# Performance work log

Measured on AMD Instinct MI355X. Metric: run time of the kernel, lower is better.

The kernel has to match this reference:

```python
import jax, jax.numpy as jnp
import numpy as np

D_HID = 1024
N_HEADS = 16
D_HEAD = D_HID // N_HEADS


def setup_inputs() -> dict:
    key = jax.random.key(0)
    k_x, k_w, k_b = jax.random.split(key, 3)
    x = jax.random.normal(k_x, (8, 4096, D_HID), dtype=jnp.float32)
    # qkv linear params (torch Linear: y = x @ W.T + b; we store W already transposed)
    W_qkv = jax.random.normal(k_w, (D_HID, 3 * D_HID), dtype=jnp.float32) / np.sqrt(D_HID)
    b_qkv = jax.random.normal(k_b, (3 * D_HID,), dtype=jnp.float32) * 0.01
    return {"x": x, "W_qkv": W_qkv, "b_qkv": b_qkv}


def reference(x, W_qkv, b_qkv):
    B, N, _ = x.shape
    qkv = x @ W_qkv + b_qkv  # [B, N, 3*d_hid]
    q, k, v = jnp.split(qkv, 3, axis=-1)

    def heads(t):  # [B, N, d_hid] -> [B, H, N, d_head]
        return t.reshape(B, N, N_HEADS, D_HEAD).transpose(0, 2, 1, 3)

    q, k, v = heads(q), heads(k), heads(v)
    # channel attention: contract over sequence N -> [B, H, d_head, d_head]
    attn = jnp.einsum("bhnd,bhne->bhde", q, k) / np.sqrt(D_HEAD)
    attn = jax.nn.softmax(attn, axis=-1)  # softmax over channel dim
    # outputs = V @ attn : [B, H, N, d_head]
    out = jnp.einsum("bhnd,bhde->bhne", v, attn)
    out = out.transpose(0, 2, 1, 3).reshape(B, N, N_HEADS * D_HEAD)
    return out
```

## Files before the change

### kernel.cpp

```cpp
#include <hip/hip_runtime.h>
#include <hip/hip_bf16.h>


typedef __attribute__((ext_vector_type(4))) float  f32x4;
typedef __attribute__((ext_vector_type(8))) short  bf16x8;
typedef __attribute__((ext_vector_type(8))) unsigned short u16x8;

typedef __attribute__((address_space(1))) const unsigned int GBUF;
typedef __attribute__((address_space(3))) unsigned int       LBUF;

#define DEVI __device__ __forceinline__

static constexpr int BATCH = 8;
static constexpr int NSEQ  = 4096;
static constexpr int DHID  = 1024;
static constexpr int NHEAD = 16;
static constexpr int DH    = 64;
static constexpr int MROWS = BATCH * NSEQ;
static constexpr int N3    = 3 * DHID;

DEVI unsigned short f2bf(float f) {
    unsigned int u = __float_as_uint(f);
    u = (u + 0x7fffu + ((u >> 16) & 1u)) >> 16;
    return (unsigned short)u;
}

__global__ void k_cvt_x(const float* __restrict__ x, unsigned short* __restrict__ xb, int n8) {
    int i = blockIdx.x * 256 + threadIdx.x;
    int stride = gridDim.x * 256;
    for (; i < n8; i += stride) {
        f32x4 a = *(const f32x4*)(x + (size_t)i * 8);
        f32x4 b = *(const f32x4*)(x + (size_t)i * 8 + 4);
        u16x8 r;
#pragma unroll
        for (int j = 0; j < 4; j++) { r[j] = f2bf(a[j]); r[4 + j] = f2bf(b[j]); }
        *(u16x8*)(xb + (size_t)i * 8) = r;
    }
}

__global__ void k_wt(const float* __restrict__ W, unsigned short* __restrict__ Wt) {
    __shared__ float s[32][33];
    int c0 = blockIdx.x * 32;
    int k0 = blockIdx.y * 32;
    int tx = threadIdx.x & 31, ty = threadIdx.x >> 5;
#pragma unroll
    for (int i = 0; i < 4; i++)
        s[ty + 8 * i][tx] = W[(size_t)(k0 + ty + 8 * i) * N3 + c0 + tx];
    __syncthreads();
#pragma unroll
    for (int i = 0; i < 4; i++)
        Wt[(size_t)(c0 + ty + 8 * i) * DHID + k0 + tx] = f2bf(s[tx][ty + 8 * i]);
}

__global__ __launch_bounds__(256, 2) void k_gemm1(
        const unsigned short* __restrict__ xb, const unsigned short* __restrict__ Wt,
        const float* __restrict__ bias,
        unsigned short* __restrict__ Q, unsigned short* __restrict__ Kw,
        unsigned short* __restrict__ V) {
    __shared__ unsigned short As[128 * 32];
    __shared__ unsigned short Bs[128 * 32];

    int nwg = gridDim.x;
    int cpx = nwg >> 3;
    int id  = blockIdx.x;
    int swz = (id & 7) * cpx + (id >> 3);
    int mt = swz / 24, nt = swz % 24;
    int m0 = mt * 128, n0 = nt * 128;

    int t = threadIdx.x, l = t & 63, w = t >> 6;
    int wr = w >> 1, wc = w & 1;

    const unsigned short* aSrc = xb + (size_t)m0 * DHID;
    const unsigned short* bSrc = Wt + (size_t)n0 * DHID;
    int srow  = l >> 2;
    int skoff = (l & 3) * 8;

    f32x4 acc[4][4] = {};

    for (int ks = 0; ks < 32; ks++) {
        int kk = ks * 32;
#pragma unroll
        for (int i = 0; i < 2; i++) {
            int r = w * 32 + i * 16 + srow;
            __builtin_amdgcn_global_load_lds(
                (GBUF*)(aSrc + (size_t)r * DHID + kk + skoff),
                (LBUF*)((char*)As + (w * 2 + i) * 1024), 16, 0, 0);
            __builtin_amdgcn_global_load_lds(
                (GBUF*)(bSrc + (size_t)r * DHID + kk + skoff),
                (LBUF*)((char*)Bs + (w * 2 + i) * 1024), 16, 0, 0);
        }
        __syncthreads();
        bf16x8 af[4], bfr[4];
#pragma unroll
        for (int m = 0; m < 4; m++)
            af[m] = *(const bf16x8*)(As + (wr * 64 + m * 16 + (l & 15)) * 32 + (l >> 4) * 8);
#pragma unroll
        for (int n = 0; n < 4; n++)
            bfr[n] = *(const bf16x8*)(Bs + (wc * 64 + n * 16 + (l & 15)) * 32 + (l >> 4) * 8);
#pragma unroll
        for (int m = 0; m < 4; m++)
#pragma unroll
            for (int n = 0; n < 4; n++)
                acc[m][n] = __builtin_amdgcn_mfma_f32_16x16x32_bf16(af[m], bfr[n], acc[m][n], 0, 0, 0);
        __syncthreads();
    }

    int hg   = (n0 + wc * 64) >> 6;
    int part = hg >> 4;
    int h    = hg & 15;
    unsigned short* dst = (part == 0) ? Q : ((part == 1) ? Kw : V);
    int b   = m0 >> 12;
    int nnb = m0 & 4095;
    unsigned short* dstp = dst + ((size_t)(b * 16 + h) * NSEQ) * DH;

#pragma unroll
    for (int n = 0; n < 4; n++) {
        int e   = n * 16 + (l & 15);
        float bv = bias[n0 + wc * 64 + n * 16 + (l & 15)];
#pragma unroll
        for (int m = 0; m < 4; m++) {
            int r0 = nnb + wr * 64 + m * 16 + (l >> 4) * 4;
#pragma unroll
            for (int j = 0; j < 4; j++)
                dstp[(size_t)(r0 + j) * DH + e] = f2bf(acc[m][n][j] + bv);
        }
    }
}

__global__ __launch_bounds__(256, 2) void k_qk(
        const unsigned short* __restrict__ Q, const unsigned short* __restrict__ K,
        float* __restrict__ part) {
    __shared__ unsigned short Qt[64 * 40];
    __shared__ unsigned short Kt[64 * 40];

    int bid = blockIdx.x;
    int bh = bid >> 2, ch = bid & 3;
    const unsigned short* Qb = Q + ((size_t)bh * NSEQ + ch * 1024) * DH;
    const unsigned short* Kb = K + ((size_t)bh * NSEQ + ch * 1024) * DH;

    int t = threadIdx.x, l = t & 63, w = t >> 6;
    int wr = w >> 1, wc = w & 1;
    int nn = t & 31;
    int dg = t >> 5;

    f32x4 acc[2][2] = {};

    for (int ns = 0; ns < 32; ns++) {
        const size_t ro = (size_t)(ns * 32 + nn) * DH + dg * 8;
        bf16x8 qv = *(const bf16x8*)(Qb + ro);
        bf16x8 kv = *(const bf16x8*)(Kb + ro);
        __syncthreads();
#pragma unroll
        for (int j = 0; j < 8; j++) {
            Qt[(dg * 8 + j) * 40 + nn] = qv[j];
            Kt[(dg * 8 + j) * 40 + nn] = kv[j];
        }
        __syncthreads();
        bf16x8 a[2], b[2];
#pragma unroll
        for (int m = 0; m < 2; m++)
            a[m] = *(const bf16x8*)(Qt + (wr * 32 + m * 16 + (l & 15)) * 40 + (l >> 4) * 8);
#pragma unroll
        for (int n = 0; n < 2; n++)
            b[n] = *(const bf16x8*)(Kt + (wc * 32 + n * 16 + (l & 15)) * 40 + (l >> 4) * 8);
#pragma unroll
        for (int m = 0; m < 2; m++)
#pragma unroll
            for (int n = 0; n < 2; n++)
                acc[m][n] = __builtin_amdgcn_mfma_f32_16x16x32_bf16(a[m], b[n], acc[m][n], 0, 0, 0);
    }

    float* P = part + ((size_t)ch * 128 + bh) * 4096;
#pragma unroll
    for (int m = 0; m < 2; m++)
#pragma unroll
        for (int n = 0; n < 2; n++)
#pragma unroll
            for (int j = 0; j < 4; j++) {
                int d = wr * 32 + m * 16 + (l >> 4) * 4 + j;
                int e = wc * 32 + n * 16 + (l & 15);
                P[d * 64 + e] = acc[m][n][j];
            }
}

__global__ void k_softmax(const float* __restrict__ part, unsigned short* __restrict__ attn_t) {
    int bh = blockIdx.x;
    int d  = threadIdx.x;
    const float* p = part + (size_t)bh * 4096 + d * 64;
    const size_t cs = (size_t)128 * 4096;
    float s[64];
#pragma unroll
    for (int e = 0; e < 64; e++)
        s[e] = (p[e] + p[cs + e] + p[2 * cs + e] + p[3 * cs + e]) * 0.125f;
    float mx = s[0];
#pragma unroll
    for (int e = 1; e < 64; e++) mx = fmaxf(mx, s[e]);
    float sum = 0.f;
#pragma unroll
    for (int e = 0; e < 64; e++) { s[e] = __expf(s[e] - mx); sum += s[e]; }
    float inv = 1.f / sum;
    unsigned short* a = attn_t + (size_t)bh * 4096;
#pragma unroll
    for (int e = 0; e < 64; e++)
        a[e * 64 + d] = f2bf(s[e] * inv);
}

__global__ __launch_bounds__(256, 2) void k_out(
        const unsigned short* __restrict__ V, const unsigned short* __restrict__ attn_t,
        float* __restrict__ out) {
    int bid = blockIdx.x;
    int bh = bid >> 4, ntile = bid & 15;
    int b = bh >> 4, h = bh & 15;
    int t = threadIdx.x, l = t & 63, w = t >> 6;
    int r0 = ntile * 256 + w * 64;

    const unsigned short* Vb = V + (size_t)bh * NSEQ * DH;
    const unsigned short* Ab = attn_t + (size_t)bh * 4096;

    bf16x8 bf[4][2];
#pragma unroll
    for (int n = 0; n < 4; n++)
#pragma unroll
        for (int ks = 0; ks < 2; ks++)
            bf[n][ks] = *(const bf16x8*)(Ab + (n * 16 + (l & 15)) * 64 + ks * 32 + (l >> 4) * 8);

    f32x4 acc[4][4] = {};
#pragma unroll
    for (int m = 0; m < 4; m++) {
        const unsigned short* vr = Vb + (size_t)(r0 + m * 16 + (l & 15)) * DH + (l >> 4) * 8;
        bf16x8 av0 = *(const bf16x8*)(vr);
        bf16x8 av1 = *(const bf16x8*)(vr + 32);
#pragma unroll
        for (int n = 0; n < 4; n++) {
            acc[m][n] = __builtin_amdgcn_mfma_f32_16x16x32_bf16(av0, bf[n][0], acc[m][n], 0, 0, 0);
            acc[m][n] = __builtin_amdgcn_mfma_f32_16x16x32_bf16(av1, bf[n][1], acc[m][n], 0, 0, 0);
        }
    }

    float* ob = out + (size_t)b * NSEQ * DHID + (size_t)h * DH;
#pragma unroll
    for (int m = 0; m < 4; m++)
#pragma unroll
        for (int n = 0; n < 4; n++)
#pragma unroll
            for (int j = 0; j < 4; j++) {
                int nn = r0 + m * 16 + (l >> 4) * 4 + j;
                int e  = n * 16 + (l & 15);
                ob[(size_t)nn * DHID + e] = acc[m][n][j];
            }
}

extern "C" void kernel_launch(void* const* d_in, const int* in_sizes, int n_in,
                              void* d_out, int out_size, void* d_ws, size_t ws_size,
                              hipStream_t stream) {
    const float* x    = (const float*)d_in[0];
    const float* W    = (const float*)d_in[1];
    const float* bias = (const float*)d_in[2];
    float* out = (float*)d_out;

    char* wsp = (char*)d_ws;
    unsigned short* xb   = (unsigned short*)(wsp);
    unsigned short* Wt   = (unsigned short*)(wsp + 67108864);
    unsigned short* Qw   = (unsigned short*)(wsp + 73400320);
    unsigned short* Kww  = (unsigned short*)(wsp + 140509184);
    unsigned short* Vw   = (unsigned short*)(wsp + 207618048);
    float*          part = (float*)(wsp + 274726912);
    unsigned short* attn = (unsigned short*)(wsp + 283115520);

    k_cvt_x<<<2048, 256, 0, stream>>>(x, xb, MROWS * DHID / 8);
    k_wt<<<dim3(N3 / 32, DHID / 32), 256, 0, stream>>>(W, Wt);
    k_gemm1<<<(MROWS / 128) * (N3 / 128), 256, 0, stream>>>(xb, Wt, bias, Qw, Kww, Vw);
    k_qk<<<128 * 4, 256, 0, stream>>>(Qw, Kww, part);
    k_softmax<<<128, 64, 0, stream>>>(part, attn);
    k_out<<<128 * 16, 256, 0, stream>>>(Vw, attn, out);
}
```

Baseline: 598.7 us.

## Rewrite QKV GEMM as 256x256 tile, 8-wave, double-buffered pipelined kernel

The QKV projection GEMM moves from 128x128 tiles with 4 waves and a single LDS buffer to 256x256 tiles with 8 waves, BK=64 and double-buffered LDS. Global-to-LDS loads for the next k-step are interleaved with MFMA sub-blocks using explicit barriers, waitcnts and s_setprio. An XOR swizzle on LDS columns is meant to avoid bank conflicts. This targets the GEMM, the dominant cost, by raising data reuse and hiding load latency. In exchange it uses 128KB of LDS and a 128-float accumulator per thread, which limits occupancy, and the hand-placed waitcnts are fragile.

```diff
diff --git a/kernel.cpp b/kernel.cpp
--- a/kernel.cpp
+++ b/kernel.cpp
@@ -52,60 +52,112 @@
         Wt[(size_t)(c0 + ty + 8 * i) * DHID + k0 + tx] = f2bf(s[tx][ty + 8 * i]);
 }
 
-__global__ __launch_bounds__(256, 2) void k_gemm1(
+__global__ __launch_bounds__(512, 2) void k_gemm1(
         const unsigned short* __restrict__ xb, const unsigned short* __restrict__ Wt,
         const float* __restrict__ bias,
         unsigned short* __restrict__ Q, unsigned short* __restrict__ Kw,
         unsigned short* __restrict__ V) {
-    __shared__ unsigned short As[128 * 32];
-    __shared__ unsigned short Bs[128 * 32];
+    __shared__ __align__(16) unsigned short As[2][16384];
+    __shared__ __align__(16) unsigned short Bs[2][16384];
 
     int nwg = gridDim.x;
     int cpx = nwg >> 3;
     int id  = blockIdx.x;
     int swz = (id & 7) * cpx + (id >> 3);
-    int mt = swz / 24, nt = swz % 24;
-    int m0 = mt * 128, n0 = nt * 128;
+    int mt = swz / 12, nt = swz % 12;
+    int m0 = mt * 256, n0 = nt * 256;
 
     int t = threadIdx.x, l = t & 63, w = t >> 6;
-    int wr = w >> 1, wc = w & 1;
+    int wr = w >> 2, wc = w & 3;
+    int lr = l & 15;
 
     const unsigned short* aSrc = xb + (size_t)m0 * DHID;
     const unsigned short* bSrc = Wt + (size_t)n0 * DHID;
-    int srow  = l >> 2;
-    int skoff = (l & 3) * 8;
-
-    f32x4 acc[4][4] = {};
-
-    for (int ks = 0; ks < 32; ks++) {
-        int kk = ks * 32;
-#pragma unroll
-        for (int i = 0; i < 2; i++) {
-            int r = w * 32 + i * 16 + srow;
-            __builtin_amdgcn_global_load_lds(
-                (GBUF*)(aSrc + (size_t)r * DHID + kk + skoff),
-                (LBUF*)((char*)As + (w * 2 + i) * 1024), 16, 0, 0);
-            __builtin_amdgcn_global_load_lds(
-                (GBUF*)(bSrc + (size_t)r * DHID + kk + skoff),
-                (LBUF*)((char*)Bs + (w * 2 + i) * 1024), 16, 0, 0);
-        }
-        __syncthreads();
-        bf16x8 af[4], bfr[4];
-#pragma unroll
-        for (int m = 0; m < 4; m++)
-            af[m] = *(const bf16x8*)(As + (wr * 64 + m * 16 + (l & 15)) * 32 + (l >> 4) * 8);
-#pragma unroll
-        for (int n = 0; n < 4; n++)
-            bfr[n] = *(const bf16x8*)(Bs + (wc * 64 + n * 16 + (l & 15)) * 32 + (l >> 4) * 8);
-#pragma unroll
-        for (int m = 0; m < 4; m++)
-#pragma unroll
-            for (int n = 0; n < 4; n++)
-                acc[m][n] = __builtin_amdgcn_mfma_f32_16x16x32_bf16(af[m], bfr[n], acc[m][n], 0, 0, 0);
-        __syncthreads();
-    }
-
-    int hg   = (n0 + wc * 64) >> 6;
+
+    int scol = ((t & 7) * 8) ^ (((t >> 5) & 1) << 4);
+    int cSwz = (((l >> 4)) * 8) ^ (((lr >> 2) & 1) << 4);
+    int aRow = wr * 128 + lr;
+    int bRow = wc * 64 + lr;
+
+#define STAGE_A(bi, kt, h) do { \
+        const unsigned short* _s = aSrc + (size_t)((h) * 128 + (t >> 3)) * DHID + (kt) * 64 + scol; \
+        unsigned short* _d = &As[bi][(h) * 8192 + t * 8]; \
+        __builtin_amdgcn_global_load_lds((GBUF*)_s, (LBUF*)_d, 16, 0, 0); \
+        __builtin_amdgcn_global_load_lds((GBUF*)(_s + 64 * DHID), (LBUF*)(_d + 4096), 16, 0, 0); \
+    } while (0)
+#define STAGE_B(bi, kt, h) do { \
+        const unsigned short* _s = bSrc + (size_t)((h) * 128 + (t >> 3)) * DHID + (kt) * 64 + scol; \
+        unsigned short* _d = &Bs[bi][(h) * 8192 + t * 8]; \
+        __builtin_amdgcn_global_load_lds((GBUF*)_s, (LBUF*)_d, 16, 0, 0); \
+        __builtin_amdgcn_global_load_lds((GBUF*)(_s + 64 * DHID), (LBUF*)(_d + 4096), 16, 0, 0); \
+    } while (0)
+#define LDA(bi, dst, mh) \
+    _Pragma("unroll") for (int m2 = 0; m2 < 4; m2++) { \
+        const unsigned short* _p = &As[bi][(aRow + (mh) * 64 + m2 * 16) * 64 + cSwz]; \
+        dst[m2][0] = *(const bf16x8*)_p; \
+        dst[m2][1] = *(const bf16x8*)(_p + 32); \
+    }
+#define LDB(bi, dst, nh) \
+    _Pragma("unroll") for (int n2 = 0; n2 < 2; n2++) { \
+        const unsigned short* _p = &Bs[bi][(bRow + (nh) * 32 + n2 * 16) * 64 + cSwz]; \
+        dst[n2][0] = *(const bf16x8*)_p; \
+        dst[n2][1] = *(const bf16x8*)(_p + 32); \
+    }
+#define MM(mh, nh, A_, B_) \
+    _Pragma("unroll") for (int m2 = 0; m2 < 4; m2++) \
+    _Pragma("unroll") for (int n2 = 0; n2 < 2; n2++) { \
+        acc[(mh)*4+m2][(nh)*2+n2] = __builtin_amdgcn_mfma_f32_16x16x32_bf16(A_[m2][0], B_[n2][0], acc[(mh)*4+m2][(nh)*2+n2], 0, 0, 0); \
+        acc[(mh)*4+m2][(nh)*2+n2] = __builtin_amdgcn_mfma_f32_16x16x32_bf16(A_[m2][1], B_[n2][1], acc[(mh)*4+m2][(nh)*2+n2], 0, 0, 0); \
+    }
+#define BAR __builtin_amdgcn_s_barrier()
+#define LGKM0 do { asm volatile("s_waitcnt lgkmcnt(0)" ::: "memory"); \
+                   __builtin_amdgcn_sched_barrier(0); } while (0)
+#define VM4 asm volatile("s_waitcnt vmcnt(4)" ::: "memory")
+#define PRIO1 __builtin_amdgcn_s_setprio(1)
+#define PRIO0 __builtin_amdgcn_s_setprio(0)
+
+    f32x4 acc[8][4] = {};
+    bf16x8 fA0[4][2], fA1[4][2], fB0[2][2], fB1[2][2];
+
+    STAGE_A(0, 0, 0); STAGE_A(0, 0, 1);
+    STAGE_B(0, 0, 0); STAGE_B(0, 0, 1);
+    STAGE_A(1, 1, 0); STAGE_A(1, 1, 1);
+    VM4;
+    BAR;
+
+#pragma unroll 1
+    for (int i = 0; i < 8; ++i) {
+        int kc1 = 2 * i + 1;
+        int kn0 = (2 * i + 2) & 15, kn1 = (2 * i + 3) & 15;
+        LDA(0, fA0, 0); LDB(0, fB0, 0); STAGE_B(1, kc1, 0);
+        BAR; LGKM0; PRIO1; MM(0, 0, fA0, fB0); PRIO0; BAR;
+
+        LDA(0, fA1, 1); STAGE_B(1, kc1, 1);
+        BAR; LGKM0; PRIO1; MM(1, 0, fA1, fB0); PRIO0; BAR;
+
+        LDB(0, fB1, 1); STAGE_A(0, kn0, 0);
+        BAR; LGKM0; PRIO1; MM(1, 1, fA1, fB1); PRIO0; BAR;
+
+        STAGE_A(0, kn0, 1);
+        BAR; PRIO1; MM(0, 1, fA0, fB1); PRIO0;
+        VM4;
+        BAR;
+        LDA(1, fA0, 0); LDB(1, fB0, 0); STAGE_B(0, kn0, 0);
+        BAR; LGKM0; PRIO1; MM(0, 0, fA0, fB0); PRIO0; BAR;
+
+        LDA(1, fA1, 1); STAGE_B(0, kn0, 1);
+        BAR; LGKM0; PRIO1; MM(1, 0, fA1, fB0); PRIO0; BAR;
+
+        LDB(1, fB1, 1); STAGE_A(1, kn1, 0);
+        BAR; LGKM0; PRIO1; MM(1, 1, fA1, fB1); PRIO0; BAR;
+
+        STAGE_A(1, kn1, 1);
+        BAR; PRIO1; MM(0, 1, fA0, fB1); PRIO0;
+        VM4;
+        BAR;
+    }
+
+    int hg   = nt * 4 + wc;
     int part = hg >> 4;
     int h    = hg & 15;
     unsigned short* dst = (part == 0) ? Q : ((part == 1) ? Kw : V);
@@ -115,16 +167,26 @@
 
 #pragma unroll
     for (int n = 0; n < 4; n++) {
-        int e   = n * 16 + (l & 15);
-        float bv = bias[n0 + wc * 64 + n * 16 + (l & 15)];
-#pragma unroll
-        for (int m = 0; m < 4; m++) {
-            int r0 = nnb + wr * 64 + m * 16 + (l >> 4) * 4;
+        int e    = n * 16 + lr;
+        float bv = bias[n0 + wc * 64 + n * 16 + lr];
+#pragma unroll
+        for (int m = 0; m < 8; m++) {
+            int r0 = nnb + wr * 128 + m * 16 + (l >> 4) * 4;
 #pragma unroll
             for (int j = 0; j < 4; j++)
                 dstp[(size_t)(r0 + j) * DH + e] = f2bf(acc[m][n][j] + bv);
         }
     }
+#undef STAGE_A
+#undef STAGE_B
+#undef LDA
+#undef LDB
+#undef MM
+#undef BAR
+#undef LGKM0
+#undef VM4
+#undef PRIO1
+#undef PRIO0
 }
 
 __global__ __launch_bounds__(256, 2) void k_qk(
@@ -269,7 +331,7 @@
 
     k_cvt_x<<<2048, 256, 0, stream>>>(x, xb, MROWS * DHID / 8);
     k_wt<<<dim3(N3 / 32, DHID / 32), 256, 0, stream>>>(W, Wt);
-    k_gemm1<<<(MROWS / 128) * (N3 / 128), 256, 0, stream>>>(xb, Wt, bias, Qw, Kww, Vw);
+    k_gemm1<<<(MROWS / 256) * (N3 / 256), 512, 0, stream>>>(xb, Wt, bias, Qw, Kww, Vw);
     k_qk<<<128 * 4, 256, 0, stream>>>(Qw, Kww, part);
     k_softmax<<<128, 64, 0, stream>>>(part, attn);
     k_out<<<128 * 16, 256, 0, stream>>>(Vw, attn, out);
```

New measurement: 631.7 us. 5.5% more time.
